# Kernel optimization log

Hardware: AMD Instinct MI355X
Metric: run time of the kernel (lower is better)

The kernel has to match this reference:

```python
import jax, jax.numpy as jnp
import numpy as np

C = 64
RED = 4            # attention reduction: conv_match C -> C//RED
CR = C // RED      # 16, also MultiScaleSpatialAttention reduced channels
N_HASHES = 4
CHUNK = 512
RES_SCALE = 0.1
EPS = 5e-5


def conv2d(x, w, b=None, padding=0, groups=1):
    out = jax.lax.conv_general_dilated(
        x, w, (1, 1), [(padding, padding), (padding, padding)],
        dimension_numbers=('NCHW', 'OIHW', 'NCHW'), feature_group_count=groups)
    if b is not None:
        out = out + b[None, :, None, None]
    return out


def ds_conv(x, pw_w, dw_w, dw_b, padding):
    # pointwise (no bias) then depthwise (bias)
    x = conv2d(x, pw_w)
    return conv2d(x, dw_w, dw_b, padding=padding, groups=dw_w.shape[0])


def pool2(x, mode):
    B, Cc, H, W = x.shape
    xr = x.reshape(B, Cc, H // 2, 2, W // 2, 2)
    return xr.max(axis=(3, 5)) if mode == 'max' else xr.mean(axis=(3, 5))


def bilinear_ac(x, out_h, out_w):
    # bilinear interpolation with align_corners=True (matches F.interpolate)
    B, Cc, h, w = x.shape
    def coords(n_in, n_out):
        pos = jnp.arange(n_out, dtype=x.dtype) * ((n_in - 1) / (n_out - 1))
        lo = jnp.floor(pos).astype(jnp.int32)
        hi = jnp.minimum(lo + 1, n_in - 1)
        frac = pos - lo.astype(x.dtype)
        return lo, hi, frac
    lo_h, hi_h, fh = coords(h, out_h)
    x = x[:, :, lo_h, :] * (1 - fh)[None, None, :, None] + x[:, :, hi_h, :] * fh[None, None, :, None]
    lo_w, hi_w, fw = coords(w, out_w)
    x = x[:, :, :, lo_w] * (1 - fw) + x[:, :, :, hi_w] * fw
    return x


def sparse_attn(x, wm, bm, wa, ba, rot):
    # NLSN-style LSH-chunked non-local sparse attention
    N, Cc, H, W = x.shape
    L = H * W
    xe = conv2d(x, wm, bm).reshape(N, -1, L).transpose(0, 2, 1)   # [N,L,Ce]
    ye = conv2d(x, wa, ba).reshape(N, -1, L).transpose(0, 2, 1)   # [N,L,C]
    Ce = xe.shape[-1]
    n_chunks = L // CHUNK                     # L multiple of CHUNK here -> no padding
    buckets = min(n_chunks + n_chunks % 2, 128)
    # LSH hashing (rot: [Ce, n_hashes, buckets//2])
    rv = jnp.einsum('blf,fhi->bhli', xe, rot)
    rv = jnp.concatenate([rv, -rv], axis=-1)  # [N,nh,L,buckets]
    codes = jnp.argmax(rv, axis=-1) + (jnp.arange(N_HASHES) * buckets)[None, :, None]
    codes = codes.reshape(N, -1)              # [N, nh*L]
    idx = jnp.argsort(codes, axis=-1)
    undo = jnp.argsort(idx, axis=-1)
    mod_idx = idx % L
    xs = jnp.take_along_axis(xe, mod_idx[:, :, None], axis=1)     # [N,nh*L,Ce]
    ys = jnp.take_along_axis(ye, mod_idx[:, :, None], axis=1)     # [N,nh*L,C]
    xb = xs.reshape(N, N_HASHES, n_chunks, CHUNK, Ce)
    yb = ys.reshape(N, N_HASHES, n_chunks, CHUNK, Cc)
    xm = xb / jnp.maximum(jnp.linalg.norm(xb, axis=-1, keepdims=True), EPS)
    def adj(t):  # add previous / next bucket (circular)
        return jnp.concatenate([t, jnp.roll(t, 1, axis=2), jnp.roll(t, -1, axis=2)], axis=3)
    xm3, yb3 = adj(xm), adj(yb)
    raw = jnp.einsum('bhkie,bhkje->bhkij', xb, xm3)               # [N,nh,k,CHUNK,3*CHUNK]
    bscore = jax.nn.logsumexp(raw, axis=-1, keepdims=True)
    score = jnp.exp(raw - bscore)
    ret = jnp.einsum('bhkij,bhkje->bhkie', score, yb3)            # [N,nh,k,CHUNK,C]
    ret = ret.reshape(N, N_HASHES * L, Cc)
    bscore = bscore.reshape(N, N_HASHES * L)
    ret = jnp.take_along_axis(ret, undo[:, :, None], axis=1).reshape(N, N_HASHES, L, Cc)
    bscore = jnp.take_along_axis(bscore, undo, axis=1).reshape(N, N_HASHES, L, 1)
    probs = jax.nn.softmax(bscore, axis=1)                        # over hash rounds
    out = (ret * probs).sum(axis=1)                               # [N,L,C]
    out = out.transpose(0, 2, 1).reshape(N, Cc, H, W)
    return out * RES_SCALE + x


def setup_inputs() -> dict:
    key = jax.random.key(0)
    ks = iter(jax.random.split(key, 40))
    w = lambda *s: jax.random.normal(next(ks), s, jnp.float32) * 0.1
    inp = {
        'x': jax.random.normal(next(ks), (2, C, 128, 128), jnp.float32),
        'spa_down_w': w(CR, C, 1, 1), 'spa_down_b': w(CR),
        's0_pw_w': w(2 * CR, CR, 1, 1), 's0_dw_w': w(2 * CR, 1, 1, 1), 's0_dw_b': w(2 * CR),
        'br3_pw_w': w(CR, CR, 1, 1), 'br3_dw_w': w(CR, 1, 3, 3), 'br3_dw_b': w(CR),
        'br5_pw_w': w(CR, CR, 1, 1), 'br5_dw_w': w(CR, 1, 5, 5), 'br5_dw_b': w(CR),
        'br7_pw_w': w(CR, CR, 1, 1), 'br7_dw_w': w(CR, 1, 7, 7), 'br7_dw_b': w(CR),
        'fusion_w': w(C, 8 * CR, 1, 1), 'fusion_b': w(C),
        'resid_w': w(C, C, 1, 1), 'resid_b': w(C),
        'ca_w1': w(C // 16, C, 1, 1), 'ca_b1': w(C // 16),
        'ca_w2': w(C, C // 16, 1, 1), 'ca_b2': w(C),
        'conv1x1_w': w(C, C, 1, 1), 'conv1x1_b': w(C),
        'match_w': w(CR, C, 1, 1), 'match_b': w(CR),
        'asm_w': w(C, C, 1, 1), 'asm_b': w(C),
        'rot': jax.random.normal(next(ks), (CR, N_HASHES, 16), jnp.float32),  # buckets//2 = 16
        'collect_w': w(C, C, 1, 1), 'collect_b': w(C),
    }
    return inp


def reference(x, spa_down_w, spa_down_b, s0_pw_w, s0_dw_w, s0_dw_b,
              br3_pw_w, br3_dw_w, br3_dw_b, br5_pw_w, br5_dw_w, br5_dw_b,
              br7_pw_w, br7_dw_w, br7_dw_b, fusion_w, fusion_b,
              resid_w, resid_b, ca_w1, ca_b1, ca_w2, ca_b2,
              conv1x1_w, conv1x1_b, match_w, match_b, asm_w, asm_b, rot,
              collect_w, collect_b):
    B, Cc, H, W = x.shape
    # --- MultiScaleSpatialAttention ---
    xr = conv2d(x, spa_down_w, spa_down_b)                # [B,16,H,W]
    s0 = ds_conv(xr, s0_pw_w, s0_dw_w, s0_dw_b, padding=0)
    feats = [s0]
    for pw, dw, db, pad in ((br3_pw_w, br3_dw_w, br3_dw_b, 1),
                            (br5_pw_w, br5_dw_w, br5_dw_b, 2),
                            (br7_pw_w, br7_dw_w, br7_dw_b, 3)):
        mx = ds_conv(pool2(xr, 'max'), pw, dw, db, pad)
        av = ds_conv(pool2(xr, 'avg'), pw, dw, db, pad)
        feats.append(jnp.concatenate([bilinear_ac(mx, H, W), bilinear_ac(av, H, W)], axis=1))
    attn = jax.nn.sigmoid(conv2d(jnp.concatenate(feats, axis=1), fusion_w, fusion_b))
    spa_mask = x * attn + conv2d(x, resid_w, resid_b)
    # --- CALayer ---
    y = x.mean(axis=(2, 3), keepdims=True)
    y = jax.nn.sigmoid(conv2d(jax.nn.relu(conv2d(y, ca_w1, ca_b1)), ca_w2, ca_b2))
    spe_mask = x * y
    # --- combine + SparseMaskConv (n_layers=1: attention then 1x1 collect) ---
    mask = conv2d(spa_mask + spe_mask, conv1x1_w, conv1x1_b) + x
    fea = sparse_attn(mask, match_w, match_b, asm_w, asm_b, rot)
    out1 = conv2d(fea, collect_w, collect_b)
    return out1 + x
```

## Files before the change

kernel.cpp:

```cpp
#include <hip/hip_runtime.h>
#include <math.h>

static constexpr int NB = 2;
static constexpr int NC = 64;
static constexpr int NHp = 128, NWp = 128;
static constexpr int NL = NHp * NWp;
static constexpr int NCR = 16;
static constexpr int NL2 = 64 * 64;
static constexpr int NHASH = 4;
static constexpr int CHUNKSZ = 512;
static constexpr int NCHUNKS = 32;
static constexpr int TOT = NHASH * NL;
static constexpr int NKEY = 128;
static constexpr int NTILE = 256;
static constexpr int TILESZ = TOT / NTILE;

typedef _Float16 half4 __attribute__((ext_vector_type(4)));
typedef _Float16 half8 __attribute__((ext_vector_type(8)));
typedef float f32x4 __attribute__((ext_vector_type(4)));

static constexpr size_t OFF_MASK = 0;
static constexpr size_t OFF_FEA  = OFF_MASK + (size_t)NB*NC*NL;
static constexpr size_t OFF_XE   = OFF_FEA  + (size_t)NB*NC*NL;
static constexpr size_t OFF_XEH  = OFF_XE   + (size_t)NB*NL*NCR;
static constexpr size_t OFF_XENH = OFF_XEH  + (size_t)NB*NL*NCR/2;
static constexpr size_t OFF_VS   = OFF_XENH + (size_t)NB*NL*NCR/2;
static constexpr size_t OFF_RET  = OFF_VS   + (size_t)NB*TOT*NC/2;
static constexpr size_t OFF_BSC  = OFF_RET  + (size_t)NB*TOT*NC/2;
static constexpr size_t OFF_INT  = OFF_BSC  + (size_t)NB*TOT;
static constexpr size_t IOFF_CODES = 0;
static constexpr size_t IOFF_IDX   = IOFF_CODES + (size_t)NB*TOT;
static constexpr size_t IOFF_UNDO  = IOFF_IDX   + (size_t)NB*TOT;
static constexpr size_t IOFF_HIST  = IOFF_UNDO  + (size_t)NB*TOT;
static constexpr size_t IOFF_OFFS  = IOFF_HIST  + (size_t)NB*NKEY*NTILE/2;
static constexpr size_t IOFF_END   = IOFF_OFFS  + (size_t)NB*NKEY*NTILE/2;
static constexpr size_t OFF_CAY = OFF_INT + IOFF_END;
static constexpr size_t OFF_CAS = OFF_CAY + 128;
static constexpr size_t OFF_CRW = OFF_CAS + 128;
static constexpr size_t OFF_CRB = OFF_CRW + 4096;
static constexpr size_t OFF_QS = OFF_FEA;
static constexpr size_t OFF_KS = OFF_QS + (size_t)NB*TOT*NCR/2;
static_assert(OFF_KS + (size_t)NB*TOT*NCR/2 <= OFF_XE, "qs/ks fit in fea region");
static constexpr size_t OFF_PMX   = OFF_FEA;
static constexpr size_t OFF_PAV   = OFF_PMX  + (size_t)NB*NCR*NL2;
static constexpr size_t OFF_PTMP  = OFF_PAV  + (size_t)NB*NCR*NL2;
static constexpr size_t OFF_DWT   = OFF_PTMP + (size_t)6*NB*NCR*NL2;
static_assert(OFF_DWT + (size_t)6*NB*NCR*NL2 <= OFF_XE, "halfres overlay fits");
static constexpr size_t OFF_XR    = OFF_XE;
static constexpr size_t OFF_FEATS = OFF_XR + (size_t)NB*NCR*NL;
static_assert(OFF_FEATS + (size_t)NB*128*NL <= OFF_RET, "feats overlay fits");
static constexpr size_t OFF_PRE1  = OFF_FEA;

__device__ __forceinline__ float sigmoidf_(float v){ return 1.0f/(1.0f + expf(-v)); }


__global__ __launch_bounds__(256,4) void k_xr(const float* __restrict__ x,
                     const float* __restrict__ w,
                     const float* __restrict__ b, float* __restrict__ xr){
  int gid = blockIdx.x*256 + threadIdx.x;
  int pix = gid >> 1, hf = gid & 1;
  int bb = pix >> 14, p = pix & (NL-1);
  const float* xi = x + (size_t)bb*NC*NL + (size_t)hf*32*NL + p;
  float acc[16];
  #pragma unroll
  for (int oc=0; oc<16; ++oc) acc[oc] = hf ? 0.f : b[oc];
  for (int ic0=0; ic0<32; ic0+=16){
    float r[16];
    #pragma unroll
    for (int j=0; j<16; ++j) r[j] = xi[(size_t)(ic0+j)*NL];
    #pragma unroll
    for (int oc=0; oc<16; ++oc){
      #pragma unroll
      for (int j=0; j<16; ++j) acc[oc] += r[j]*w[oc*64 + hf*32 + ic0 + j];
    }
  }
  #pragma unroll
  for (int oc=0; oc<16; ++oc) acc[oc] += __shfl_xor(acc[oc], 1, 64);
  if (!hf){
    float* xo = xr + (size_t)bb*NCR*NL + p;
    #pragma unroll
    for (int oc=0; oc<16; ++oc) xo[(size_t)oc*NL] = acc[oc];
  }
}

__global__ __launch_bounds__(256,4) void k_s0(const float* __restrict__ xr,
                     const float* __restrict__ pw,
                     const float* __restrict__ dww, const float* __restrict__ dwb,
                     float* __restrict__ feats){
  int gid = blockIdx.x*256 + threadIdx.x;
  int oc0 = blockIdx.y*16;
  int bb = gid >> 14, p = gid & (NL-1);
  const float* xi = xr + (size_t)bb*NCR*NL + p;
  float r[16];
  #pragma unroll
  for (int ic=0; ic<16; ++ic) r[ic] = xi[(size_t)ic*NL];
  float* fo = feats + (size_t)bb*128*NL + p;
  #pragma unroll
  for (int j=0; j<16; ++j){
    int oc = oc0 + j;
    float s = 0.f;
    #pragma unroll
    for (int ic=0; ic<16; ++ic) s += r[ic]*pw[oc*16+ic];
    fo[(size_t)oc*NL] = s*dww[oc] + dwb[oc];
  }
}

__global__ void k_pool(const float* __restrict__ xr, float* __restrict__ pmax,
                       float* __restrict__ pavg){
  int gid = blockIdx.x*256 + threadIdx.x;
  if (gid >= NB*NCR*NL2) return;
  int p = gid & (NL2-1); int t = gid >> 12; int c = t & 15; int bb = t >> 4;
  int y = p >> 6, x2 = p & 63;
  const float* base = xr + (size_t)(bb*NCR + c)*NL + (size_t)(2*y)*NWp + 2*x2;
  float a = base[0], b_ = base[1], c_ = base[NWp], d = base[NWp+1];
  pmax[gid] = fmaxf(fmaxf(a,b_), fmaxf(c_,d));
  pavg[gid] = 0.25f*(a+b_+c_+d);
}

__global__ void k_pw16_all(const float* __restrict__ pmx, const float* __restrict__ pav,
                           const float* __restrict__ w0, const float* __restrict__ w1,
                           const float* __restrict__ w2, float* __restrict__ out){
  int gid = blockIdx.x*256 + threadIdx.x;
  if (gid >= 6*NB*NL2) return;
  int p = gid & (NL2-1); int t = gid >> 12; int bb = t & 1; int combo = t >> 1;
  int br = combo >> 1, mode = combo & 1;
  const float* w = (br==0) ? w0 : (br==1) ? w1 : w2;
  const float* in = ((mode==0) ? pmx : pav) + (size_t)bb*NCR*NL2 + p;
  float r[16];
  #pragma unroll
  for (int ic=0; ic<16; ++ic) r[ic] = in[(size_t)ic*NL2];
  float* oo = out + ((size_t)(combo*NB + bb)*NCR)*NL2 + p;
  #pragma unroll
  for (int oc=0; oc<16; ++oc){
    float s = 0.f;
    #pragma unroll
    for (int ic=0; ic<16; ++ic) s += r[ic]*w[oc*16+ic];
    oo[(size_t)oc*NL2] = s;
  }
}

__global__ void k_dw_all(const float* __restrict__ in,
                         const float* __restrict__ w3, const float* __restrict__ b3,
                         const float* __restrict__ w5, const float* __restrict__ b5,
                         const float* __restrict__ w7, const float* __restrict__ b7,
                         float* __restrict__ out){
  int gid = blockIdx.x*256 + threadIdx.x;
  if (gid >= 6*NB*NCR*NL2) return;
  int p = gid & (NL2-1); int t = gid >> 12; int c = t & 15; int r2 = t >> 4;
  int bb = r2 & 1; int combo = r2 >> 1;
  int br = combo >> 1;
  int K = (br==0) ? 3 : (br==1) ? 5 : 7; int P = K >> 1;
  const float* w = (br==0) ? w3 : (br==1) ? w5 : w7;
  const float* bias = (br==0) ? b3 : (br==1) ? b5 : b7;
  int y = p >> 6, x = p & 63;
  const float* xi = in + ((size_t)(combo*NB + bb)*NCR + c)*NL2;
  float s = bias[c];
  for (int dy=0; dy<K; ++dy){
    int iy = y + dy - P;
    if ((unsigned)iy < 64u){
      for (int dx=0; dx<K; ++dx){
        int ix = x + dx - P;
        if ((unsigned)ix < 64u) s += xi[iy*64 + ix] * w[(c*K + dy)*K + dx];
      }
    }
  }
  out[gid] = s;
}

__global__ void k_up_all(const float* __restrict__ in, float* __restrict__ feats){
  int gid = blockIdx.x*256 + threadIdx.x;
  if (gid >= 6*NB*NCR*NL) return;
  int p = gid & (NL-1); int t = gid >> 14; int c = t & 15; int r2 = t >> 4;
  int bb = r2 & 1; int combo = r2 >> 1;
  int y = p >> 7, x = p & 127;
  const float sc = 63.0f/127.0f;
  float fy = y*sc; int ly = (int)floorf(fy); int hy = min(ly+1, 63); fy -= (float)ly;
  float fx = x*sc; int lx = (int)floorf(fx); int hx = min(lx+1, 63); float gx = fx - (float)lx;
  const float* xi = in + ((size_t)(combo*NB + bb)*NCR + c)*NL2;
  float v0 = xi[ly*64+lx]*(1.f-fy) + xi[hy*64+lx]*fy;
  float v1 = xi[ly*64+hx]*(1.f-fy) + xi[hy*64+hx]*fy;
  int coff = 32 + combo*16 + c;
  feats[(size_t)bb*128*NL + (size_t)coff*NL + p] = v0*(1.f-gx) + v1*gx;
}

__global__ void k_camean(const float* __restrict__ x, float* __restrict__ cay){
  __shared__ float red[256];
  int bc = blockIdx.x; int tid = threadIdx.x;
  float s = 0.f;
  for (int i = tid; i < NL; i += 256) s += x[(size_t)bc*NL + i];
  red[tid] = s; __syncthreads();
  for (int st=128; st>0; st>>=1){ if (tid<st) red[tid]+=red[tid+st]; __syncthreads(); }
  if (tid==0) cay[bc] = red[0] / (float)NL;
}

__global__ void k_camlp(const float* __restrict__ cay,
                        const float* __restrict__ w1, const float* __restrict__ b1,
                        const float* __restrict__ w2, const float* __restrict__ b2,
                        float* __restrict__ cas){
  __shared__ float z[NB*4];
  int tid = threadIdx.x;
  if (tid < NB*4){
    int bb = tid >> 2, j = tid & 3;
    float s = b1[j];
    for (int ic=0; ic<NC; ++ic) s += cay[bb*NC+ic]*w1[j*NC+ic];
    z[tid] = fmaxf(s, 0.f);
  }
  __syncthreads();
  if (tid < NB*NC){
    int bb = tid >> 6, oc = tid & 63;
    float s = b2[oc];
    #pragma unroll
    for (int j=0; j<4; ++j) s += z[bb*4+j]*w2[oc*4+j];
    cas[tid] = sigmoidf_(s);
  }
}

__global__ void k_wprod(const float* __restrict__ c11w, const float* __restrict__ c11b,
                        const float* __restrict__ rw, const float* __restrict__ rb,
                        float* __restrict__ crw, float* __restrict__ crb){
  int gid = blockIdx.x*256 + threadIdx.x;
  if (gid >= 4096) return;
  int o = gid >> 6, i = gid & 63;
  float s = 0.f;
  for (int k=0; k<64; ++k) s += c11w[o*64+k]*rw[k*64+i];
  crw[gid] = s;
  if (i == 0){
    float t = c11b[o];
    for (int k=0; k<64; ++k) t += c11w[o*64+k]*rb[k];
    crb[o] = t;
  }
}

__global__ __launch_bounds__(256,4) void k_attnmul(const float* __restrict__ x,
                          const float* __restrict__ feats,
                          const float* __restrict__ fw, const float* __restrict__ fb,
                          const float* __restrict__ cas, float* __restrict__ pre1){
  int gid = blockIdx.x*256 + threadIdx.x;
  int oc0 = blockIdx.y*16;
  int bb = gid >> 14, p = gid & (NL-1);
  const float* fi = feats + (size_t)bb*128*NL + p;
  float acc[16];
  #pragma unroll
  for (int j=0; j<16; ++j) acc[j] = fb[oc0+j];
  for (int k0=0; k0<128; k0+=8){
    float fr[8];
    #pragma unroll
    for (int j=0; j<8; ++j) fr[j] = fi[(size_t)(k0+j)*NL];
    #pragma unroll
    for (int j=0; j<16; ++j){
      #pragma unroll
      for (int t=0; t<8; ++t) acc[j] += fr[t]*fw[(oc0+j)*128+k0+t];
    }
  }
  const float* xb = x + (size_t)bb*NC*NL + p;
  float* po = pre1 + (size_t)bb*NC*NL + p;
  #pragma unroll
  for (int j=0; j<16; ++j){
    int oc = oc0 + j;
    float xv = xb[(size_t)oc*NL];
    po[(size_t)oc*NL] = xv*(sigmoidf_(acc[j]) + cas[bb*64+oc]);
  }
}

__global__ __launch_bounds__(256,4) void k_mask(const float* __restrict__ pre1,
                       const float* __restrict__ c11w,
                       const float* __restrict__ crw, const float* __restrict__ crb,
                       const float* __restrict__ x, float* __restrict__ mask){
  int gid = blockIdx.x*256 + threadIdx.x;
  int oc0 = blockIdx.y*16;
  int bb = gid >> 14, p = gid & (NL-1);
  const float* pi = pre1 + (size_t)bb*NC*NL + p;
  const float* xi = x + (size_t)bb*NC*NL + p;
  float acc[16];
  #pragma unroll
  for (int j=0; j<16; ++j) acc[j] = crb[oc0+j];
  for (int ic0=0; ic0<64; ic0+=8){
    float pr[8], xr8[8];
    #pragma unroll
    for (int j=0; j<8; ++j){ pr[j] = pi[(size_t)(ic0+j)*NL]; xr8[j] = xi[(size_t)(ic0+j)*NL]; }
    #pragma unroll
    for (int j=0; j<16; ++j){
      #pragma unroll
      for (int t=0; t<8; ++t)
        acc[j] += pr[t]*c11w[(oc0+j)*64+ic0+t] + xr8[t]*crw[(oc0+j)*64+ic0+t];
    }
  }
  float* mo = mask + (size_t)bb*NC*NL + p;
  #pragma unroll
  for (int j=0; j<16; ++j){
    int oc = oc0 + j;
    mo[(size_t)oc*NL] = acc[j] + xi[(size_t)oc*NL];
  }
}


__global__ __launch_bounds__(256,4) void k_xe(const float* __restrict__ mask,
                     const float* __restrict__ w, const float* __restrict__ b,
                     const float* __restrict__ rot,
                     _Float16* __restrict__ xeh, _Float16* __restrict__ xenh,
                     int* __restrict__ codes, int* __restrict__ hist){
  int gid = blockIdx.x*256 + threadIdx.x;
  int pix = gid >> 1, hf = gid & 1;
  int bb = pix >> 14, l = pix & (NL-1);
  const float* mi = mask + (size_t)bb*NC*NL + (size_t)hf*32*NL + l;
  float acc[16];
  #pragma unroll
  for (int oc=0; oc<16; ++oc) acc[oc] = hf ? 0.f : b[oc];
  for (int ic0=0; ic0<32; ic0+=16){
    float r[16];
    #pragma unroll
    for (int j=0; j<16; ++j) r[j] = mi[(size_t)(ic0+j)*NL];
    #pragma unroll
    for (int oc=0; oc<16; ++oc){
      #pragma unroll
      for (int j=0; j<16; ++j) acc[oc] += r[j]*w[oc*64 + hf*32 + ic0 + j];
    }
  }
  #pragma unroll
  for (int oc=0; oc<16; ++oc) acc[oc] += __shfl_xor(acc[oc], 1, 64);
  if (!hf){
    float n2 = 0.f;
    #pragma unroll
    for (int oc=0; oc<16; ++oc) n2 += acc[oc]*acc[oc];
    float inv = 1.0f / fmaxf(sqrtf(n2), 5e-5f);
    _Float16* ho = xeh + (size_t)pix*NCR;
    _Float16* no = xenh + (size_t)pix*NCR;
    #pragma unroll
    for (int g=0; g<4; ++g){
      half4 hv, nv;
      #pragma unroll
      for (int j=0; j<4; ++j){ hv[j] = (_Float16)acc[g*4+j]; nv[j] = (_Float16)(acc[g*4+j]*inv); }
      *(half4*)(ho + g*4) = hv;
      *(half4*)(no + g*4) = nv;
    }
  }
  #pragma unroll
  for (int hh=0; hh<2; ++hh){
    int h = hf*2 + hh;
    float rv[16];
    #pragma unroll
    for (int i=0; i<16; ++i){
      float s = 0.f;
      #pragma unroll
      for (int f=0; f<16; ++f) s += acc[f]*rot[(f*NHASH + h)*16 + i];
      rv[i] = s;
    }
    float best = -1e30f; int bi = 0;
    #pragma unroll
    for (int i=0; i<16; ++i){ if (rv[i] > best){ best = rv[i]; bi = i; } }
    #pragma unroll
    for (int i=0; i<16; ++i){ float val = -rv[i]; if (val > best){ best = val; bi = 16+i; } }
    int code = bi + h*32;
    codes[((bb*NHASH + h) << 14) + l] = code;
    int tile = h*64 + (l >> 8);
    atomicAdd(&hist[bb*NKEY*NTILE + code*NTILE + tile], 1);
  }
}

__global__ __launch_bounds__(256,4) void k_yeh(const float* __restrict__ mask,
                      const float* __restrict__ w, const float* __restrict__ b,
                      const int* __restrict__ undo, _Float16* __restrict__ vs){
  int gid = blockIdx.x*256 + threadIdx.x;
  int oc0 = blockIdx.y*16;
  int bb = gid >> 14, l = gid & (NL-1);
  const float* mi = mask + (size_t)bb*NC*NL + l;
  float acc[16];
  #pragma unroll
  for (int j=0; j<16; ++j) acc[j] = b[oc0+j];
  for (int ic0=0; ic0<64; ic0+=8){
    float r[8];
    #pragma unroll
    for (int j=0; j<8; ++j) r[j] = mi[(size_t)(ic0+j)*NL];
    #pragma unroll
    for (int j=0; j<16; ++j){
      #pragma unroll
      for (int t=0; t<8; ++t) acc[j] += r[t]*w[(oc0+j)*64+ic0+t];
    }
  }
  half8 h0, h1;
  #pragma unroll
  for (int j=0; j<8; ++j){ h0[j] = (_Float16)acc[j]; h1[j] = (_Float16)acc[8+j]; }
  const int* ub = undo + bb*TOT;
  #pragma unroll
  for (int h=0; h<4; ++h){
    int pos = ub[h*NL + l];
    _Float16* vo = vs + ((size_t)bb*TOT + pos)*64 + oc0;
    *(half8*)(vo) = h0;
    *(half8*)(vo + 8) = h1;
  }
}

__global__ __launch_bounds__(256,4) void k_gather(const int* __restrict__ idx,
                      const _Float16* __restrict__ xeh, const _Float16* __restrict__ xenh,
                      _Float16* __restrict__ qs, _Float16* __restrict__ ks){
  int gid = blockIdx.x*256 + threadIdx.x;
  int pos = gid >> 1, hf = gid & 1;
  int bb = pos >> 16;
  int p = pos & (TOT-1);
  int l = idx[bb*TOT + p] & (NL-1);
  *(half8*)(qs + (size_t)pos*16 + hf*8) = *(const half8*)(xeh + ((size_t)bb*NL + l)*16 + hf*8);
  *(half8*)(ks + (size_t)pos*16 + hf*8) = *(const half8*)(xenh + ((size_t)bb*NL + l)*16 + hf*8);
}

__global__ void k_scan(const int* __restrict__ hist, int* __restrict__ offs){
  __shared__ int part[256];
  int bb = blockIdx.x; int t = threadIdx.x;
  const int* hi = hist + (size_t)bb*NKEY*NTILE;
  int* oo = offs + (size_t)bb*NKEY*NTILE;
  int s = 0;
  for (int i=0; i<128; ++i) s += hi[t*128 + i];
  part[t] = s; __syncthreads();
  int v = s;
  for (int off=1; off<256; off<<=1){
    int u = (t >= off) ? part[t-off] : 0;
    __syncthreads();
    v += u; part[t] = v;
    __syncthreads();
  }
  int run = v - s;
  for (int i=0; i<128; ++i){ int q = hi[t*128+i]; oo[t*128+i] = run; run += q; }
}

__global__ __launch_bounds__(256) void k_scatter(const int* __restrict__ codes,
                          const int* __restrict__ offs,
                          int* __restrict__ idx, int* __restrict__ undo){
  __shared__ int cnt[4][NKEY];
  int wid = threadIdx.x >> 6, lane = threadIdx.x & 63;
  int t4 = blockIdx.x;
  int bb = t4 >> 6;
  int tile = (t4 & 63)*4 + wid;
  cnt[wid][lane] = 0; cnt[wid][64+lane] = 0;
  const int* cb = codes + bb*TOT;
  const int* ob = offs + (size_t)bb*NKEY*NTILE;
  int* ib = idx + bb*TOT;
  int* ub = undo + bb*TOT;
  for (int g=0; g<4; ++g){
    int j = tile*TILESZ + g*64 + lane;
    int k = cb[j];
    unsigned long long m = ~0ull;
    #pragma unroll
    for (int bit=0; bit<7; ++bit){
      unsigned long long bmask = __ballot((k >> bit) & 1);
      m &= ((k >> bit) & 1) ? bmask : ~bmask;
    }
    int rank = __popcll(m & ((1ull << lane) - 1ull));
    int leader = __ffsll((unsigned long long)m) - 1;
    int base = 0;
    if (lane == leader){
      base = cnt[wid][k];
      cnt[wid][k] = base + __popcll(m);
    }
    base = __shfl(base, leader, 64);
    int pos = ob[k*NTILE + tile] + base + rank;
    ib[pos] = j;
    ub[j] = pos;
    __threadfence_block();
  }
}

__global__ __launch_bounds__(512) void k_attn(
    const _Float16* __restrict__ qs, const _Float16* __restrict__ ks,
    const _Float16* __restrict__ vs,
    _Float16* __restrict__ retb, float* __restrict__ bsc){
  __shared__ _Float16 kt[64*20];
  __shared__ _Float16 vt[64*70];
  int blk = blockIdx.x;
  int qh = blk & 1; int kk = (blk >> 1) & 31; int h = (blk >> 6) & 3; int bb = blk >> 8;
  int tid = threadIdx.x;
  int w = tid >> 6, lane = tid & 63, col = lane & 15, grp = lane >> 4;
  int qbase = h*NL + kk*CHUNKSZ + qh*256 + w*32;

  half4 qfr[2]; int posq[2];
  #pragma unroll
  for (int qf=0; qf<2; ++qf){
    posq[qf] = qbase + qf*16 + col;
    qfr[qf] = *(const half4*)(qs + ((size_t)bb*TOT + posq[qf])*16 + grp*4);
  }

  f32x4 O[4][2];
  #pragma unroll
  for (int a=0; a<4; ++a)
    #pragma unroll
    for (int b=0; b<2; ++b) O[a][b] = (f32x4){0.f,0.f,0.f,0.f};
  float m_[2] = {-1e30f,-1e30f};
  float ssum[2] = {0.f,0.f};

  for (int t=0; t<24; ++t){
    __syncthreads();
    {
      int kx = tid & 63, c0 = (tid >> 6) * 8;
      int jj = t*64 + kx; int sec = jj >> 9; int j0 = jj & 511;
      int cc = kk + ((sec==1) ? -1 : (sec==2) ? 1 : 0);
      cc = (cc + NCHUNKS) & (NCHUNKS-1);
      int spos = h*NL + cc*CHUNKSZ + j0;
      half8 vv = *(const half8*)(vs + ((size_t)bb*TOT + spos)*64 + c0);
      #pragma unroll
      for (int j=0; j<8; ++j) vt[(c0+j)*70 + kx] = vv[j];
    }
    if (tid < 128){
      int r = tid >> 1, hf = tid & 1;
      int jj = t*64 + r; int sec = jj >> 9; int j0 = jj & 511;
      int cc = kk + ((sec==1) ? -1 : (sec==2) ? 1 : 0);
      cc = (cc + NCHUNKS) & (NCHUNKS-1);
      int spos = h*NL + cc*CHUNKSZ + j0;
      *(half8*)(kt + r*20 + hf*8) =
          *(const half8*)(ks + ((size_t)bb*TOT + spos)*16 + hf*8);
    }
    __syncthreads();

    f32x4 S[4][2];
    #pragma unroll
    for (int kb=0; kb<4; ++kb){
      half4 ka = *(const half4*)(kt + (kb*16 + col)*20 + grp*4);
      #pragma unroll
      for (int qf=0; qf<2; ++qf)
        S[kb][qf] = __builtin_amdgcn_mfma_f32_16x16x16f16(
            ka, qfr[qf], (f32x4){0.f,0.f,0.f,0.f}, 0, 0, 0);
    }

    half4 pf[2][4];
    #pragma unroll
    for (int qf=0; qf<2; ++qf){
      float mtl = -1e30f;
      #pragma unroll
      for (int kb=0; kb<4; ++kb)
        #pragma unroll
        for (int i=0; i<4; ++i) mtl = fmaxf(mtl, S[kb][qf][i]);
      if (__any(mtl > m_[qf] + 8.0f)){
        float mt = fmaxf(mtl, __shfl_xor(mtl, 16, 64));
        mt = fmaxf(mt, __shfl_xor(mt, 32, 64));
        float mn = fmaxf(m_[qf], mt);
        float sc = __expf(m_[qf] - mn);
        ssum[qf] *= sc;
        m_[qf] = mn;
        #pragma unroll
        for (int cf=0; cf<4; ++cf)
          #pragma unroll
          for (int i=0; i<4; ++i) O[cf][qf][i] *= sc;
      }
      float ps = 0.f;
      #pragma unroll
      for (int kb=0; kb<4; ++kb){
        #pragma unroll
        for (int i=0; i<4; ++i){
          float p = __expf(S[kb][qf][i] - m_[qf]);
          ps += p;
          pf[qf][kb][i] = (_Float16)p;
        }
      }
      ssum[qf] += ps;
    }

    #pragma unroll
    for (int cf=0; cf<4; ++cf){
      #pragma unroll
      for (int k2=0; k2<2; ++k2){
        half4 a0 = *(const half4*)(vt + (cf*16 + col)*70 + k2*32 + grp*4);
        half4 a1 = *(const half4*)(vt + (cf*16 + col)*70 + k2*32 + 16 + grp*4);
        half8 va;
        #pragma unroll
        for (int i=0; i<4; ++i){ va[i] = a0[i]; va[4+i] = a1[i]; }
        #pragma unroll
        for (int qf=0; qf<2; ++qf){
          half8 pb;
          #pragma unroll
          for (int i=0; i<4; ++i){ pb[i] = pf[qf][2*k2][i]; pb[4+i] = pf[qf][2*k2+1][i]; }
          O[cf][qf] = __builtin_amdgcn_mfma_f32_16x16x32_f16(
              va, pb, O[cf][qf], 0, 0, 0);
        }
      }
    }
  }

  #pragma unroll
  for (int qf=0; qf<2; ++qf){
    float st = ssum[qf];
    st += __shfl_xor(st, 16, 64);
    st += __shfl_xor(st, 32, 64);
    float inv = 1.0f/st;
    size_t rb = ((size_t)bb*TOT + posq[qf])*64;
    #pragma unroll
    for (int cf=0; cf<4; ++cf){
      half4 o;
      #pragma unroll
      for (int i=0; i<4; ++i) o[i] = (_Float16)(O[cf][qf][i]*inv);
      *(half4*)(retb + rb + cf*16 + grp*4) = o;
    }
    if (grp == 0) bsc[(size_t)bb*TOT + posq[qf]] = m_[qf] + logf(st);
  }
}

__global__ __launch_bounds__(256,4) void k_combine(const _Float16* __restrict__ retb,
                          const float* __restrict__ bsc,
                          const int* __restrict__ undo, const float* __restrict__ mask,
                          float* __restrict__ fea){
  int gid = blockIdx.x*256 + threadIdx.x;
  int c0 = blockIdx.y*32;
  int bb = gid >> 14; int l = gid & (NL-1);
  const int* ub = undo + bb*TOT;
  int pos[4]; float sc[4];
  #pragma unroll
  for (int h=0; h<4; ++h){ pos[h] = ub[h*NL + l]; sc[h] = bsc[bb*TOT + pos[h]]; }
  float mx = fmaxf(fmaxf(sc[0],sc[1]), fmaxf(sc[2],sc[3]));
  float e[4]; float tot = 0.f;
  #pragma unroll
  for (int h=0; h<4; ++h){ e[h] = __expf(sc[h]-mx); tot += e[h]; }
  float inv = 0.1f/tot;
  const float* mb_ = mask + (size_t)bb*NC*NL + l;
  float* fo = fea + (size_t)bb*NC*NL + l;
  const _Float16* r0 = retb + ((size_t)bb*TOT + pos[0])*NC + c0;
  const _Float16* r1 = retb + ((size_t)bb*TOT + pos[1])*NC + c0;
  const _Float16* r2 = retb + ((size_t)bb*TOT + pos[2])*NC + c0;
  const _Float16* r3 = retb + ((size_t)bb*TOT + pos[3])*NC + c0;
  #pragma unroll
  for (int g=0; g<4; ++g){
    half8 v0 = *(const half8*)(r0 + g*8);
    half8 v1 = *(const half8*)(r1 + g*8);
    half8 v2 = *(const half8*)(r2 + g*8);
    half8 v3 = *(const half8*)(r3 + g*8);
    #pragma unroll
    for (int j=0; j<8; ++j){
      int c = c0 + g*8 + j;
      float v = (float)v0[j]*e[0] + (float)v1[j]*e[1] + (float)v2[j]*e[2] + (float)v3[j]*e[3];
      fo[(size_t)c*NL] = v*inv + mb_[(size_t)c*NL];
    }
  }
}

__global__ __launch_bounds__(256,4) void k_collect(const float* __restrict__ fea,
                          const float* __restrict__ w,
                          const float* __restrict__ b, const float* __restrict__ x,
                          float* __restrict__ out){
  int gid = blockIdx.x*256 + threadIdx.x;
  int oc0 = blockIdx.y*16;
  int bb = gid >> 14, p = gid & (NL-1);
  const float* fi = fea + (size_t)bb*NC*NL + p;
  const float* xi = x + (size_t)bb*NC*NL + p;
  float acc[16];
  #pragma unroll
  for (int j=0; j<16; ++j) acc[j] = b[oc0+j];
  for (int ic0=0; ic0<64; ic0+=8){
    float r[8];
    #pragma unroll
    for (int j=0; j<8; ++j) r[j] = fi[(size_t)(ic0+j)*NL];
    #pragma unroll
    for (int j=0; j<16; ++j){
      #pragma unroll
      for (int t=0; t<8; ++t) acc[j] += r[t]*w[(oc0+j)*64+ic0+t];
    }
  }
  float* oo = out + (size_t)bb*NC*NL + p;
  #pragma unroll
  for (int j=0; j<16; ++j){
    int oc = oc0 + j;
    oo[(size_t)oc*NL] = acc[j] + xi[(size_t)oc*NL];
  }
}

extern "C" void kernel_launch(void* const* d_in, const int* in_sizes, int n_in,
                              void* d_out, int out_size, void* d_ws, size_t ws_size,
                              hipStream_t stream) {
  const float* x        = (const float*)d_in[0];
  const float* spa_dw   = (const float*)d_in[1];
  const float* spa_db   = (const float*)d_in[2];
  const float* s0_pw    = (const float*)d_in[3];
  const float* s0_dww   = (const float*)d_in[4];
  const float* s0_dwb   = (const float*)d_in[5];
  const float* fus_w    = (const float*)d_in[15];
  const float* fus_b    = (const float*)d_in[16];
  const float* res_w    = (const float*)d_in[17];
  const float* res_b    = (const float*)d_in[18];
  const float* ca_w1    = (const float*)d_in[19];
  const float* ca_b1    = (const float*)d_in[20];
  const float* ca_w2    = (const float*)d_in[21];
  const float* ca_b2    = (const float*)d_in[22];
  const float* c11_w    = (const float*)d_in[23];
  const float* c11_b    = (const float*)d_in[24];
  const float* match_w  = (const float*)d_in[25];
  const float* match_b  = (const float*)d_in[26];
  const float* asm_w    = (const float*)d_in[27];
  const float* asm_b    = (const float*)d_in[28];
  const float* rot      = (const float*)d_in[29];
  const float* col_w    = (const float*)d_in[30];
  const float* col_b    = (const float*)d_in[31];
  float* out = (float*)d_out;

  float* ws    = (float*)d_ws;
  float* mask  = ws + OFF_MASK;
  float* fea   = ws + OFF_FEA;
  _Float16* xeh  = (_Float16*)(ws + OFF_XEH);
  _Float16* xenh = (_Float16*)(ws + OFF_XENH);
  _Float16* vsort = (_Float16*)(ws + OFF_VS);
  _Float16* qsort = (_Float16*)(ws + OFF_QS);
  _Float16* ksort = (_Float16*)(ws + OFF_KS);
  _Float16* retb = (_Float16*)(ws + OFF_RET);
  float* bsc   = ws + OFF_BSC;
  int*   ib    = (int*)(ws + OFF_INT);
  int* codes   = ib + IOFF_CODES;
  int* idx     = ib + IOFF_IDX;
  int* undo    = ib + IOFF_UNDO;
  int* hist    = ib + IOFF_HIST;
  int* offs    = ib + IOFF_OFFS;
  float* cay   = ws + OFF_CAY;
  float* cas   = ws + OFF_CAS;
  float* crw   = ws + OFF_CRW;
  float* crb   = ws + OFF_CRB;
  float* xr    = ws + OFF_XR;
  float* feats = ws + OFF_FEATS;
  float* pmx   = ws + OFF_PMX;
  float* pav   = ws + OFF_PAV;
  float* ptmp  = ws + OFF_PTMP;
  float* dwt   = ws + OFF_DWT;
  float* pre1  = ws + OFF_PRE1;

  k_xr<<<(NB*NL*2)/256, 256, 0, stream>>>(x, spa_dw, spa_db, xr);
  k_wprod<<<16, 256, 0, stream>>>(c11_w, c11_b, res_w, res_b, crw, crb);
  k_s0<<<dim3((NB*NL)/256, 2), 256, 0, stream>>>(xr, s0_pw, s0_dww, s0_dwb, feats);
  k_pool<<<(NB*NCR*NL2)/256, 256, 0, stream>>>(xr, pmx, pav);
  k_pw16_all<<<(6*NB*NL2)/256, 256, 0, stream>>>(pmx, pav,
      (const float*)d_in[6], (const float*)d_in[9], (const float*)d_in[12], ptmp);
  k_dw_all<<<(6*NB*NCR*NL2)/256, 256, 0, stream>>>(ptmp,
      (const float*)d_in[7], (const float*)d_in[8],
      (const float*)d_in[10], (const float*)d_in[11],
      (const float*)d_in[13], (const float*)d_in[14], dwt);
  k_up_all<<<(6*NB*NCR*NL)/256, 256, 0, stream>>>(dwt, feats);
  k_camean<<<NB*NC, 256, 0, stream>>>(x, cay);
  k_camlp<<<1, 128, 0, stream>>>(cay, ca_w1, ca_b1, ca_w2, ca_b2, cas);
  k_attnmul<<<dim3((NB*NL)/256, 4), 256, 0, stream>>>(x, feats, fus_w, fus_b, cas, pre1);
  k_mask<<<dim3((NB*NL)/256, 4), 256, 0, stream>>>(pre1, c11_w, crw, crb, x, mask);

  hipMemsetAsync(hist, 0, (size_t)NB*NKEY*NTILE*sizeof(int), stream);
  k_xe<<<(NB*NL*2)/256, 256, 0, stream>>>(mask, match_w, match_b, rot, xeh, xenh, codes, hist);
  k_scan<<<NB, 256, 0, stream>>>(hist, offs);
  k_scatter<<<NB*NTILE/4, 256, 0, stream>>>(codes, offs, idx, undo);
  k_yeh<<<dim3((NB*NL)/256, 4), 256, 0, stream>>>(mask, asm_w, asm_b, undo, vsort);
  k_gather<<<(NB*TOT*2)/256, 256, 0, stream>>>(idx, xeh, xenh, qsort, ksort);
  k_attn<<<NB*NHASH*NCHUNKS*2, 512, 0, stream>>>(qsort, ksort, vsort, retb, bsc);
  k_combine<<<dim3((NB*NL)/256, 2), 256, 0, stream>>>(retb, bsc, undo, mask, fea);
  k_collect<<<dim3((NB*NL)/256, 4), 256, 0, stream>>>(fea, col_w, col_b, x, out);
}
```

Baseline: 328.6 us.

## Fuse pooling into pointwise, gather into scatter, widen 1x1 convs, prefetch attention tiles

Folds the 2x2 max/avg pooling into the pointwise branch kernel and the q/k gather into the scatter kernel, removing two launches and their intermediate buffers. The 1x1 conv kernels (attnmul, mask, yeh, collect) now compute 32 output channels per thread instead of 16, so each input element is loaded half as often, at the cost of more registers and lower occupancy bounds. The attention kernel prefetches the next V/K tile into registers before the compute of the current tile, and packs the probabilities directly into half8 MFMA operands.

```diff
diff --git a/kernel.cpp b/kernel.cpp
--- a/kernel.cpp
+++ b/kernel.cpp
@@ -41,9 +41,7 @@
 static constexpr size_t OFF_QS = OFF_FEA;
 static constexpr size_t OFF_KS = OFF_QS + (size_t)NB*TOT*NCR/2;
 static_assert(OFF_KS + (size_t)NB*TOT*NCR/2 <= OFF_XE, "qs/ks fit in fea region");
-static constexpr size_t OFF_PMX   = OFF_FEA;
-static constexpr size_t OFF_PAV   = OFF_PMX  + (size_t)NB*NCR*NL2;
-static constexpr size_t OFF_PTMP  = OFF_PAV  + (size_t)NB*NCR*NL2;
+static constexpr size_t OFF_PTMP  = OFF_FEA;
 static constexpr size_t OFF_DWT   = OFF_PTMP + (size_t)6*NB*NCR*NL2;
 static_assert(OFF_DWT + (size_t)6*NB*NCR*NL2 <= OFF_XE, "halfres overlay fits");
 static constexpr size_t OFF_XR    = OFF_XE;
@@ -105,19 +103,7 @@
   }
 }
 
-__global__ void k_pool(const float* __restrict__ xr, float* __restrict__ pmax,
-                       float* __restrict__ pavg){
-  int gid = blockIdx.x*256 + threadIdx.x;
-  if (gid >= NB*NCR*NL2) return;
-  int p = gid & (NL2-1); int t = gid >> 12; int c = t & 15; int bb = t >> 4;
-  int y = p >> 6, x2 = p & 63;
-  const float* base = xr + (size_t)(bb*NCR + c)*NL + (size_t)(2*y)*NWp + 2*x2;
-  float a = base[0], b_ = base[1], c_ = base[NWp], d = base[NWp+1];
-  pmax[gid] = fmaxf(fmaxf(a,b_), fmaxf(c_,d));
-  pavg[gid] = 0.25f*(a+b_+c_+d);
-}
-
-__global__ void k_pw16_all(const float* __restrict__ pmx, const float* __restrict__ pav,
+__global__ void k_pw16_all(const float* __restrict__ xr,
                            const float* __restrict__ w0, const float* __restrict__ w1,
                            const float* __restrict__ w2, float* __restrict__ out){
   int gid = blockIdx.x*256 + threadIdx.x;
@@ -125,10 +111,14 @@
   int p = gid & (NL2-1); int t = gid >> 12; int bb = t & 1; int combo = t >> 1;
   int br = combo >> 1, mode = combo & 1;
   const float* w = (br==0) ? w0 : (br==1) ? w1 : w2;
-  const float* in = ((mode==0) ? pmx : pav) + (size_t)bb*NCR*NL2 + p;
+  int y = p >> 6, x2 = p & 63;
   float r[16];
   #pragma unroll
-  for (int ic=0; ic<16; ++ic) r[ic] = in[(size_t)ic*NL2];
+  for (int ic=0; ic<16; ++ic){
+    const float* base = xr + (size_t)(bb*NCR + ic)*NL + (size_t)(2*y)*NWp + 2*x2;
+    float a = base[0], b_ = base[1], c_ = base[NWp], d = base[NWp+1];
+    r[ic] = mode ? 0.25f*(a+b_+c_+d) : fmaxf(fmaxf(a,b_), fmaxf(c_,d));
+  }
   float* oo = out + ((size_t)(combo*NB + bb)*NCR)*NL2 + p;
   #pragma unroll
   for (int oc=0; oc<16; ++oc){
@@ -231,23 +221,23 @@
   }
 }
 
-__global__ __launch_bounds__(256,4) void k_attnmul(const float* __restrict__ x,
+__global__ __launch_bounds__(256,3) void k_attnmul(const float* __restrict__ x,
                           const float* __restrict__ feats,
                           const float* __restrict__ fw, const float* __restrict__ fb,
                           const float* __restrict__ cas, float* __restrict__ pre1){
   int gid = blockIdx.x*256 + threadIdx.x;
-  int oc0 = blockIdx.y*16;
+  int oc0 = blockIdx.y*32;
   int bb = gid >> 14, p = gid & (NL-1);
   const float* fi = feats + (size_t)bb*128*NL + p;
-  float acc[16];
-  #pragma unroll
-  for (int j=0; j<16; ++j) acc[j] = fb[oc0+j];
+  float acc[32];
+  #pragma unroll
+  for (int j=0; j<32; ++j) acc[j] = fb[oc0+j];
   for (int k0=0; k0<128; k0+=8){
     float fr[8];
     #pragma unroll
     for (int j=0; j<8; ++j) fr[j] = fi[(size_t)(k0+j)*NL];
     #pragma unroll
-    for (int j=0; j<16; ++j){
+    for (int j=0; j<32; ++j){
       #pragma unroll
       for (int t=0; t<8; ++t) acc[j] += fr[t]*fw[(oc0+j)*128+k0+t];
     }
@@ -255,31 +245,31 @@
   const float* xb = x + (size_t)bb*NC*NL + p;
   float* po = pre1 + (size_t)bb*NC*NL + p;
   #pragma unroll
-  for (int j=0; j<16; ++j){
+  for (int j=0; j<32; ++j){
     int oc = oc0 + j;
     float xv = xb[(size_t)oc*NL];
     po[(size_t)oc*NL] = xv*(sigmoidf_(acc[j]) + cas[bb*64+oc]);
   }
 }
 
-__global__ __launch_bounds__(256,4) void k_mask(const float* __restrict__ pre1,
+__global__ __launch_bounds__(256,3) void k_mask(const float* __restrict__ pre1,
                        const float* __restrict__ c11w,
                        const float* __restrict__ crw, const float* __restrict__ crb,
                        const float* __restrict__ x, float* __restrict__ mask){
   int gid = blockIdx.x*256 + threadIdx.x;
-  int oc0 = blockIdx.y*16;
+  int oc0 = blockIdx.y*32;
   int bb = gid >> 14, p = gid & (NL-1);
   const float* pi = pre1 + (size_t)bb*NC*NL + p;
   const float* xi = x + (size_t)bb*NC*NL + p;
-  float acc[16];
-  #pragma unroll
-  for (int j=0; j<16; ++j) acc[j] = crb[oc0+j];
+  float acc[32];
+  #pragma unroll
+  for (int j=0; j<32; ++j) acc[j] = crb[oc0+j];
   for (int ic0=0; ic0<64; ic0+=8){
     float pr[8], xr8[8];
     #pragma unroll
     for (int j=0; j<8; ++j){ pr[j] = pi[(size_t)(ic0+j)*NL]; xr8[j] = xi[(size_t)(ic0+j)*NL]; }
     #pragma unroll
-    for (int j=0; j<16; ++j){
+    for (int j=0; j<32; ++j){
       #pragma unroll
       for (int t=0; t<8; ++t)
         acc[j] += pr[t]*c11w[(oc0+j)*64+ic0+t] + xr8[t]*crw[(oc0+j)*64+ic0+t];
@@ -287,7 +277,7 @@
   }
   float* mo = mask + (size_t)bb*NC*NL + p;
   #pragma unroll
-  for (int j=0; j<16; ++j){
+  for (int j=0; j<32; ++j){
     int oc = oc0 + j;
     mo[(size_t)oc*NL] = acc[j] + xi[(size_t)oc*NL];
   }
@@ -357,49 +347,39 @@
   }
 }
 
-__global__ __launch_bounds__(256,4) void k_yeh(const float* __restrict__ mask,
+__global__ __launch_bounds__(256,3) void k_yeh(const float* __restrict__ mask,
                       const float* __restrict__ w, const float* __restrict__ b,
                       const int* __restrict__ undo, _Float16* __restrict__ vs){
   int gid = blockIdx.x*256 + threadIdx.x;
-  int oc0 = blockIdx.y*16;
+  int oc0 = blockIdx.y*32;
   int bb = gid >> 14, l = gid & (NL-1);
   const float* mi = mask + (size_t)bb*NC*NL + l;
-  float acc[16];
-  #pragma unroll
-  for (int j=0; j<16; ++j) acc[j] = b[oc0+j];
+  float acc[32];
+  #pragma unroll
+  for (int j=0; j<32; ++j) acc[j] = b[oc0+j];
   for (int ic0=0; ic0<64; ic0+=8){
     float r[8];
     #pragma unroll
     for (int j=0; j<8; ++j) r[j] = mi[(size_t)(ic0+j)*NL];
     #pragma unroll
-    for (int j=0; j<16; ++j){
+    for (int j=0; j<32; ++j){
       #pragma unroll
       for (int t=0; t<8; ++t) acc[j] += r[t]*w[(oc0+j)*64+ic0+t];
     }
   }
-  half8 h0, h1;
-  #pragma unroll
-  for (int j=0; j<8; ++j){ h0[j] = (_Float16)acc[j]; h1[j] = (_Float16)acc[8+j]; }
+  half8 hv[4];
+  #pragma unroll
+  for (int g=0; g<4; ++g)
+    #pragma unroll
+    for (int j=0; j<8; ++j) hv[g][j] = (_Float16)acc[g*8+j];
   const int* ub = undo + bb*TOT;
   #pragma unroll
   for (int h=0; h<4; ++h){
     int pos = ub[h*NL + l];
     _Float16* vo = vs + ((size_t)bb*TOT + pos)*64 + oc0;
-    *(half8*)(vo) = h0;
-    *(half8*)(vo + 8) = h1;
-  }
-}
-
-__global__ __launch_bounds__(256,4) void k_gather(const int* __restrict__ idx,
-                      const _Float16* __restrict__ xeh, const _Float16* __restrict__ xenh,
-                      _Float16* __restrict__ qs, _Float16* __restrict__ ks){
-  int gid = blockIdx.x*256 + threadIdx.x;
-  int pos = gid >> 1, hf = gid & 1;
-  int bb = pos >> 16;
-  int p = pos & (TOT-1);
-  int l = idx[bb*TOT + p] & (NL-1);
-  *(half8*)(qs + (size_t)pos*16 + hf*8) = *(const half8*)(xeh + ((size_t)bb*NL + l)*16 + hf*8);
-  *(half8*)(ks + (size_t)pos*16 + hf*8) = *(const half8*)(xenh + ((size_t)bb*NL + l)*16 + hf*8);
+    #pragma unroll
+    for (int g=0; g<4; ++g) *(half8*)(vo + g*8) = hv[g];
+  }
 }
 
 __global__ void k_scan(const int* __restrict__ hist, int* __restrict__ offs){
@@ -423,7 +403,9 @@
 
 __global__ __launch_bounds__(256) void k_scatter(const int* __restrict__ codes,
                           const int* __restrict__ offs,
-                          int* __restrict__ idx, int* __restrict__ undo){
+                          const _Float16* __restrict__ xeh, const _Float16* __restrict__ xenh,
+                          int* __restrict__ idx, int* __restrict__ undo,
+                          _Float16* __restrict__ qs, _Float16* __restrict__ ks){
   __shared__ int cnt[4][NKEY];
   int wid = threadIdx.x >> 6, lane = threadIdx.x & 63;
   int t4 = blockIdx.x;
@@ -454,6 +436,15 @@
     int pos = ob[k*NTILE + tile] + base + rank;
     ib[pos] = j;
     ub[j] = pos;
+    int l = j & (NL-1);
+    const _Float16* qp = xeh + ((size_t)bb*NL + l)*16;
+    const _Float16* kp = xenh + ((size_t)bb*NL + l)*16;
+    _Float16* qo = qs + ((size_t)bb*TOT + pos)*16;
+    _Float16* ko = ks + ((size_t)bb*TOT + pos)*16;
+    *(half8*)(qo)     = *(const half8*)(qp);
+    *(half8*)(qo + 8) = *(const half8*)(qp + 8);
+    *(half8*)(ko)     = *(const half8*)(kp);
+    *(half8*)(ko + 8) = *(const half8*)(kp + 8);
     __threadfence_block();
   }
 }
@@ -485,28 +476,28 @@
   float m_[2] = {-1e30f,-1e30f};
   float ssum[2] = {0.f,0.f};
 
+  int kx = tid & 63, c0 = (tid >> 6) * 8;
+  int kr = tid >> 1, khf = tid & 1;
+
+  #define SPOS(jj) ({ int sec_ = (jj) >> 9; int j0_ = (jj) & 511; \
+      int cc_ = kk + ((sec_==1) ? -1 : (sec_==2) ? 1 : 0); \
+      cc_ = (cc_ + NCHUNKS) & (NCHUNKS-1); h*NL + cc_*CHUNKSZ + j0_; })
+
+  half8 vv = *(const half8*)(vs + ((size_t)bb*TOT + SPOS(kx))*64 + c0);
+  half8 kv;
+  if (tid < 128) kv = *(const half8*)(ks + ((size_t)bb*TOT + SPOS(kr))*16 + khf*8);
+
   for (int t=0; t<24; ++t){
     __syncthreads();
-    {
-      int kx = tid & 63, c0 = (tid >> 6) * 8;
-      int jj = t*64 + kx; int sec = jj >> 9; int j0 = jj & 511;
-      int cc = kk + ((sec==1) ? -1 : (sec==2) ? 1 : 0);
-      cc = (cc + NCHUNKS) & (NCHUNKS-1);
-      int spos = h*NL + cc*CHUNKSZ + j0;
-      half8 vv = *(const half8*)(vs + ((size_t)bb*TOT + spos)*64 + c0);
-      #pragma unroll
-      for (int j=0; j<8; ++j) vt[(c0+j)*70 + kx] = vv[j];
-    }
-    if (tid < 128){
-      int r = tid >> 1, hf = tid & 1;
-      int jj = t*64 + r; int sec = jj >> 9; int j0 = jj & 511;
-      int cc = kk + ((sec==1) ? -1 : (sec==2) ? 1 : 0);
-      cc = (cc + NCHUNKS) & (NCHUNKS-1);
-      int spos = h*NL + cc*CHUNKSZ + j0;
-      *(half8*)(kt + r*20 + hf*8) =
-          *(const half8*)(ks + ((size_t)bb*TOT + spos)*16 + hf*8);
-    }
+    #pragma unroll
+    for (int j=0; j<8; ++j) vt[(c0+j)*70 + kx] = vv[j];
+    if (tid < 128) *(half8*)(kt + kr*20 + khf*8) = kv;
     __syncthreads();
+    if (t+1 < 24){
+      int jj = (t+1)*64;
+      vv = *(const half8*)(vs + ((size_t)bb*TOT + SPOS(jj + kx))*64 + c0);
+      if (tid < 128) kv = *(const half8*)(ks + ((size_t)bb*TOT + SPOS(jj + kr))*16 + khf*8);
+    }
 
     f32x4 S[4][2];
     #pragma unroll
@@ -518,7 +509,7 @@
             ka, qfr[qf], (f32x4){0.f,0.f,0.f,0.f}, 0, 0, 0);
     }
 
-    half4 pf[2][4];
+    half8 pb[2][2];
     #pragma unroll
     for (int qf=0; qf<2; ++qf){
       float mtl = -1e30f;
@@ -540,13 +531,17 @@
       }
       float ps = 0.f;
       #pragma unroll
-      for (int kb=0; kb<4; ++kb){
+      for (int k2=0; k2<2; ++k2){
+        half8 hb;
         #pragma unroll
         for (int i=0; i<4; ++i){
-          float p = __expf(S[kb][qf][i] - m_[qf]);
-          ps += p;
-          pf[qf][kb][i] = (_Float16)p;
+          float p0 = __expf(S[2*k2][qf][i]   - m_[qf]);
+          float p1 = __expf(S[2*k2+1][qf][i] - m_[qf]);
+          ps += p0 + p1;
+          hb[i]   = (_Float16)p0;
+          hb[4+i] = (_Float16)p1;
         }
+        pb[qf][k2] = hb;
       }
       ssum[qf] += ps;
     }
@@ -561,16 +556,13 @@
         #pragma unroll
         for (int i=0; i<4; ++i){ va[i] = a0[i]; va[4+i] = a1[i]; }
         #pragma unroll
-        for (int qf=0; qf<2; ++qf){
-          half8 pb;
-          #pragma unroll
-          for (int i=0; i<4; ++i){ pb[i] = pf[qf][2*k2][i]; pb[4+i] = pf[qf][2*k2+1][i]; }
+        for (int qf=0; qf<2; ++qf)
           O[cf][qf] = __builtin_amdgcn_mfma_f32_16x16x32_f16(
-              va, pb, O[cf][qf], 0, 0, 0);
-        }
+              va, pb[qf][k2], O[cf][qf], 0, 0, 0);
       }
     }
   }
+  #undef SPOS
 
   #pragma unroll
   for (int qf=0; qf<2; ++qf){
@@ -627,31 +619,31 @@
   }
 }
 
-__global__ __launch_bounds__(256,4) void k_collect(const float* __restrict__ fea,
+__global__ __launch_bounds__(256,3) void k_collect(const float* __restrict__ fea,
                           const float* __restrict__ w,
                           const float* __restrict__ b, const float* __restrict__ x,
                           float* __restrict__ out){
   int gid = blockIdx.x*256 + threadIdx.x;
-  int oc0 = blockIdx.y*16;
+  int oc0 = blockIdx.y*32;
   int bb = gid >> 14, p = gid & (NL-1);
   const float* fi = fea + (size_t)bb*NC*NL + p;
   const float* xi = x + (size_t)bb*NC*NL + p;
-  float acc[16];
-  #pragma unroll
-  for (int j=0; j<16; ++j) acc[j] = b[oc0+j];
+  float acc[32];
+  #pragma unroll
+  for (int j=0; j<32; ++j) acc[j] = b[oc0+j];
   for (int ic0=0; ic0<64; ic0+=8){
     float r[8];
     #pragma unroll
     for (int j=0; j<8; ++j) r[j] = fi[(size_t)(ic0+j)*NL];
     #pragma unroll
-    for (int j=0; j<16; ++j){
+    for (int j=0; j<32; ++j){
       #pragma unroll
       for (int t=0; t<8; ++t) acc[j] += r[t]*w[(oc0+j)*64+ic0+t];
     }
   }
   float* oo = out + (size_t)bb*NC*NL + p;
   #pragma unroll
-  for (int j=0; j<16; ++j){
+  for (int j=0; j<32; ++j){
     int oc = oc0 + j;
     oo[(size_t)oc*NL] = acc[j] + xi[(size_t)oc*NL];
   }
@@ -707,8 +699,6 @@
   float* crb   = ws + OFF_CRB;
   float* xr    = ws + OFF_XR;
   float* feats = ws + OFF_FEATS;
-  float* pmx   = ws + OFF_PMX;
-  float* pav   = ws + OFF_PAV;
   float* ptmp  = ws + OFF_PTMP;
   float* dwt   = ws + OFF_DWT;
   float* pre1  = ws + OFF_PRE1;
@@ -716,8 +706,7 @@
   k_xr<<<(NB*NL*2)/256, 256, 0, stream>>>(x, spa_dw, spa_db, xr);
   k_wprod<<<16, 256, 0, stream>>>(c11_w, c11_b, res_w, res_b, crw, crb);
   k_s0<<<dim3((NB*NL)/256, 2), 256, 0, stream>>>(xr, s0_pw, s0_dww, s0_dwb, feats);
-  k_pool<<<(NB*NCR*NL2)/256, 256, 0, stream>>>(xr, pmx, pav);
-  k_pw16_all<<<(6*NB*NL2)/256, 256, 0, stream>>>(pmx, pav,
+  k_pw16_all<<<(6*NB*NL2)/256, 256, 0, stream>>>(xr,
       (const float*)d_in[6], (const float*)d_in[9], (const float*)d_in[12], ptmp);
   k_dw_all<<<(6*NB*NCR*NL2)/256, 256, 0, stream>>>(ptmp,
       (const float*)d_in[7], (const float*)d_in[8],
@@ -726,16 +715,15 @@
   k_up_all<<<(6*NB*NCR*NL)/256, 256, 0, stream>>>(dwt, feats);
   k_camean<<<NB*NC, 256, 0, stream>>>(x, cay);
   k_camlp<<<1, 128, 0, stream>>>(cay, ca_w1, ca_b1, ca_w2, ca_b2, cas);
-  k_attnmul<<<dim3((NB*NL)/256, 4), 256, 0, stream>>>(x, feats, fus_w, fus_b, cas, pre1);
-  k_mask<<<dim3((NB*NL)/256, 4), 256, 0, stream>>>(pre1, c11_w, crw, crb, x, mask);
-
-  hipMemsetAsync(hist, 0, (size_t)NB*NKEY*NTILE*sizeof(int), stream);
+  k_attnmul<<<dim3((NB*NL)/256, 2), 256, 0, stream>>>(x, feats, fus_w, fus_b, cas, pre1);
+  k_mask<<<dim3((NB*NL)/256, 2), 256, 0, stream>>>(pre1, c11_w, crw, crb, x, mask);
+
+  (void)hipMemsetAsync(hist, 0, (size_t)NB*NKEY*NTILE*sizeof(int), stream);
   k_xe<<<(NB*NL*2)/256, 256, 0, stream>>>(mask, match_w, match_b, rot, xeh, xenh, codes, hist);
   k_scan<<<NB, 256, 0, stream>>>(hist, offs);
-  k_scatter<<<NB*NTILE/4, 256, 0, stream>>>(codes, offs, idx, undo);
-  k_yeh<<<dim3((NB*NL)/256, 4), 256, 0, stream>>>(mask, asm_w, asm_b, undo, vsort);
-  k_gather<<<(NB*TOT*2)/256, 256, 0, stream>>>(idx, xeh, xenh, qsort, ksort);
+  k_scatter<<<NB*NTILE/4, 256, 0, stream>>>(codes, offs, xeh, xenh, idx, undo, qsort, ksort);
+  k_yeh<<<dim3((NB*NL)/256, 2), 256, 0, stream>>>(mask, asm_w, asm_b, undo, vsort);
   k_attn<<<NB*NHASH*NCHUNKS*2, 512, 0, stream>>>(qsort, ksort, vsort, retb, bsc);
   k_combine<<<dim3((NB*NL)/256, 2), 256, 0, stream>>>(retb, bsc, undo, mask, fea);
-  k_collect<<<dim3((NB*NL)/256, 4), 256, 0, stream>>>(fea, col_w, col_b, x, out);
-}
+  k_collect<<<dim3((NB*NL)/256, 2), 256, 0, stream>>>(fea, col_w, col_b, x, out);
+}
```

Result: slower. 397.2 us (+20.9%).
